# Performance work log

Measured on AMD Instinct MI355X. Metric: run time of the kernel, lower is better.

Reference implementation:

```python
import jax, jax.numpy as jnp
import numpy as np

B, D = 8192, 8          # batch, number of input features (= number of TT cores)
P = 10                  # poly_deg + 1 (basis width per feature)
R = 512                 # fixed TT rank
OUT = 64                # output dim (dims[0])
N_MID = D - 2           # middle cores
U_LO, U_HI = -0.1, 0.1  # uniform init range


def setup_inputs() -> dict:
    key = jax.random.key(0)
    kz, k0, km, kl = jax.random.split(key, 4)
    z = jax.random.normal(kz, (B, D), dtype=jnp.float32)
    G0 = jax.random.uniform(k0, (P, R), minval=U_LO, maxval=U_HI, dtype=jnp.float32)
    G_mid = jax.random.uniform(km, (N_MID, R, P, R), minval=U_LO, maxval=U_HI, dtype=jnp.float32)
    G_last = jax.random.uniform(kl, (R, P, OUT), minval=U_LO, maxval=U_HI, dtype=jnp.float32)
    return {"z": z, "G0": G0, "G_mid": G_mid, "G_last": G_last, "t": 0}


def _poly_basis(z, p):
    # Phi[i] = [z_i^0, ..., z_i^(p-1)]  -> stacked as [B, D, P]
    return z[:, :, None] ** jnp.arange(p, dtype=z.dtype)


def reference(z, G0, G_mid, G_last, t):
    phi = _poly_basis(z, G0.shape[0])                 # [B, D, P]
    # first core: tanh(G0)[j, r], Phi0[b, j] -> res[b, r]
    res = jnp.einsum('jr,bj->br', jnp.tanh(G0), phi[:, 0, :])
    # middle cores: res[b,i] . tanh(G)[i,j,k] . Phi[b,j] -> [b,k]
    for i in range(G_mid.shape[0]):
        tmp = jnp.einsum('bi,ijk->bjk', res, jnp.tanh(G_mid[i]))   # [B, P, R]
        res = jnp.einsum('bjk,bj->bk', tmp, phi[:, i + 1, :])      # [B, R]
    # last core -> output dim
    tmp = jnp.einsum('bi,ijl->bjl', res, jnp.tanh(G_last))         # [B, P, OUT]
    res = jnp.einsum('bjl,bj->bl', tmp, phi[:, -1, :])             # [B, OUT]
    return res
```

## Files before the change

kernel.cpp:

```cpp
#include <hip/hip_runtime.h>
#include <hip/hip_bf16.h>
#include <stdint.h>

#define BB   8192
#define DD   8
#define PP   10
#define RR   512
#define OUTD 64
#define KK   5120

typedef __bf16 bf16x8 __attribute__((ext_vector_type(8)));
typedef float  f32x4  __attribute__((ext_vector_type(4)));

template <int N>
__global__ __launch_bounds__(256) void frag_pack(
        const float* __restrict__ G, __hip_bfloat16* __restrict__ dst, int ldi) {
    constexpr int LOGN = (N == 512) ? 9 : 6;
    __shared__ __hip_bfloat16 sT[32 * (N + 8)];
    const int kc = blockIdx.x, j = blockIdx.y, c = blockIdx.z;
    const float* Gp = G + (size_t)c * 512 * ldi;
    __hip_bfloat16* db = dst + (size_t)c * 5120 * N + (size_t)(j * 16 + kc) * 32 * N;
    #pragma unroll
    for (int e = 0; e < N / 32; ++e) {
        const int idx = (e * 256 + threadIdx.x) * 4;
        const int row = idx >> LOGN, col = idx & (N - 1);
        f32x4 v = *(const f32x4*)(Gp + (size_t)(kc * 32 + row) * ldi + (size_t)j * N + col);
        __hip_bfloat16* sp = sT + row * (N + 8) + col;
        sp[0] = __float2bfloat16(tanhf(v.x));
        sp[1] = __float2bfloat16(tanhf(v.y));
        sp[2] = __float2bfloat16(tanhf(v.z));
        sp[3] = __float2bfloat16(tanhf(v.w));
    }
    __syncthreads();
    #pragma unroll
    for (int cc = 0; cc < N / 64; ++cc) {
        const int ch = cc * 256 + threadIdx.x;
        const int nt = ch >> 6, l = ch & 63;
        const int r0 = (l >> 4) * 8, cb = nt * 16 + (l & 15);
        union { __hip_bfloat16 h[8]; uint4 u; } pk;
        #pragma unroll
        for (int e = 0; e < 8; ++e) pk.h[e] = sT[(r0 + e) * (N + 8) + cb];
        *(uint4*)(db + (size_t)ch * 8) = pk.u;
    }
}

__global__ __launch_bounds__(512) void tanh_g0(
        const float* __restrict__ G0, float* __restrict__ tG0) {
    const int i = blockIdx.x * 512 + threadIdx.x;
    tG0[i] = tanhf(G0[i]);
}

__global__ __launch_bounds__(512) void tt_first(
        const float* __restrict__ z, const float* __restrict__ tG0,
        __hip_bfloat16* __restrict__ res0) {
    const int r = threadIdx.x;
    const int b0 = blockIdx.x * 32;
    float tg[10];
    #pragma unroll
    for (int j = 0; j < 10; ++j) tg[j] = tG0[j * RR + r];
    #pragma unroll 1
    for (int b = 0; b < 32; ++b) {
        const float z0 = z[(size_t)(b0 + b) * DD];
        float acc = tg[9];
        #pragma unroll
        for (int j = 8; j >= 0; --j) acc = acc * z0 + tg[j];
        res0[(size_t)(b0 + b) * RR + r] = __float2bfloat16(acc);
    }
}

template <bool LASTV, int NTOT>
__global__ __launch_bounds__(256, 2) void tt_gemm_ks(
        const __hip_bfloat16* __restrict__ resin,
        const __hip_bfloat16* __restrict__ tBf,
        void* __restrict__ outp,
        const float* __restrict__ z, int d) {
    __shared__ f32x4 red[2][16][64];

    const int tid  = threadIdx.x;
    const int lane = tid & 63;
    const int wave = tid >> 6;
    const int m0 = blockIdx.x * 64;
    const int nb = blockIdx.y;
    const int r16 = lane & 15, quad = lane >> 4;

    bf16x8 a[16];
    #pragma unroll
    for (int ms = 0; ms < 4; ++ms)
        #pragma unroll
        for (int kst = 0; kst < 4; ++kst)
            a[ms * 4 + kst] = *(const bf16x8*)(
                resin + (size_t)(m0 + ms * 16 + r16) * RR + wave * 128 + kst * 32 + quad * 8);

    float zr[16];
    #pragma unroll
    for (int ms = 0; ms < 4; ++ms)
        #pragma unroll
        for (int r = 0; r < 4; ++r)
            zr[ms * 4 + r] = z[(size_t)(m0 + ms * 16 + quad * 4 + r) * DD + d];

    f32x4 acc[4][4];
    #pragma unroll
    for (int ms = 0; ms < 4; ++ms)
        #pragma unroll
        for (int sn = 0; sn < 4; ++sn) acc[ms][sn] = f32x4{0.f, 0.f, 0.f, 0.f};

    constexpr size_t SK = (size_t)NTOT * 512;
    constexpr size_t PJ = 16 * SK;
    const __hip_bfloat16* pB = tBf + (size_t)nb * 4 * 512
                             + (size_t)wave * 4 * SK + (size_t)lane * 8;

    bf16x8 bv[4][4];
    #pragma unroll
    for (int s = 0; s < 3; ++s)
        #pragma unroll
        for (int sn = 0; sn < 4; ++sn)
            bv[s][sn] = *(const bf16x8*)(pB + (size_t)9 * PJ + (size_t)s * SK + sn * 512);

#define MFMA_STEP(SLOT)                                                        \
    _Pragma("unroll")                                                          \
    for (int ms = 0; ms < 4; ++ms)                                             \
        _Pragma("unroll")                                                      \
        for (int sn = 0; sn < 4; ++sn)                                         \
            acc[ms][sn] = __builtin_amdgcn_mfma_f32_16x16x32_bf16(             \
                a[ms * 4 + SLOT], bv[SLOT][sn], acc[ms][sn], 0, 0, 0);

    #pragma unroll 1
    for (int p = 0; p < 10; ++p) {
        const int j = 9 - p;
        if (p) {
            #pragma unroll
            for (int ms = 0; ms < 4; ++ms)
                #pragma unroll
                for (int sn = 0; sn < 4; ++sn)
                    #pragma unroll
                    for (int r = 0; r < 4; ++r)
                        acc[ms][sn][r] *= zr[ms * 4 + r];
        }
        const size_t jb = (size_t)j * PJ;
        #pragma unroll
        for (int sn = 0; sn < 4; ++sn)
            bv[3][sn] = *(const bf16x8*)(pB + jb + (size_t)3 * SK + sn * 512);
        MFMA_STEP(0)
        if (p < 9) {
            #pragma unroll
            for (int sn = 0; sn < 4; ++sn)
                bv[0][sn] = *(const bf16x8*)(pB + jb - PJ + sn * 512);
        }
        MFMA_STEP(1)
        if (p < 9) {
            #pragma unroll
            for (int sn = 0; sn < 4; ++sn)
                bv[1][sn] = *(const bf16x8*)(pB + jb - PJ + SK + sn * 512);
        }
        MFMA_STEP(2)
        if (p < 9) {
            #pragma unroll
            for (int sn = 0; sn < 4; ++sn)
                bv[2][sn] = *(const bf16x8*)(pB + jb - PJ + 2 * SK + sn * 512);
        }
        MFMA_STEP(3)
    }
#undef MFMA_STEP

    if (wave & 1) {
        const int idx = wave >> 1;
        #pragma unroll
        for (int i = 0; i < 16; ++i) red[idx][i][lane] = acc[i >> 2][i & 3];
    }
    __syncthreads();
    if (wave == 0) {
        #pragma unroll
        for (int i = 0; i < 16; ++i) acc[i >> 2][i & 3] += red[0][i][lane];
    }
    if (wave == 2) {
        #pragma unroll
        for (int i = 0; i < 16; ++i) {
            f32x4 t = acc[i >> 2][i & 3] + red[1][i][lane];
            red[1][i][lane] = t;
        }
    }
    __syncthreads();
    float* rc = (float*)&red[0][0][0];
    if (wave == 0) {
        #pragma unroll
        for (int i = 0; i < 16; ++i) acc[i >> 2][i & 3] += red[1][i][lane];
        #pragma unroll
        for (int ms = 0; ms < 4; ++ms)
            #pragma unroll
            for (int sn = 0; sn < 4; ++sn)
                #pragma unroll
                for (int r = 0; r < 4; ++r)
                    rc[(ms * 16 + quad * 4 + r) * 64 + sn * 16 + r16] = acc[ms][sn][r];
    }
    __syncthreads();

    const int row = tid >> 2, cg = (tid & 3) * 16;
    if (LASTV) {
        float* o = (float*)outp;
        #pragma unroll
        for (int q = 0; q < 4; ++q)
            *(f32x4*)(o + (size_t)(m0 + row) * OUTD + cg + q * 4) =
                *(const f32x4*)(rc + row * 64 + cg + q * 4);
    } else {
        __hip_bfloat16* o = (__hip_bfloat16*)outp;
        #pragma unroll
        for (int h = 0; h < 2; ++h) {
            union { __hip_bfloat16 hh[8]; uint4 u; } pk;
            #pragma unroll
            for (int e = 0; e < 8; ++e)
                pk.hh[e] = __float2bfloat16(rc[row * 64 + cg + h * 8 + e]);
            *(uint4*)(o + (size_t)(m0 + row) * RR + nb * 64 + cg + h * 8) = pk.u;
        }
    }
}

extern "C" void kernel_launch(void* const* d_in, const int* in_sizes, int n_in,
                              void* d_out, int out_size, void* d_ws, size_t ws_size,
                              hipStream_t stream) {
    const float* z     = (const float*)d_in[0];
    const float* G0    = (const float*)d_in[1];
    const float* Gmid  = (const float*)d_in[2];
    const float* Glast = (const float*)d_in[3];
    float* out = (float*)d_out;

    char* ws = (char*)d_ws;
    __hip_bfloat16* resX   = (__hip_bfloat16*)ws;
    __hip_bfloat16* resY   = (__hip_bfloat16*)(ws + ((size_t)8 << 20));
    __hip_bfloat16* tBf    = (__hip_bfloat16*)(ws + ((size_t)16 << 20));
    __hip_bfloat16* tBlf   = (__hip_bfloat16*)(ws + ((size_t)48 << 20));
    float* tG0             = (float*)(ws + ((size_t)52 << 20));

    frag_pack<512><<<dim3(16, 10, 6), 256, 0, stream>>>(Gmid,  tBf,  PP * RR);
    frag_pack<64> <<<dim3(16, 10, 1), 256, 0, stream>>>(Glast, tBlf, PP * OUTD);
    tanh_g0<<<dim3(10), 512, 0, stream>>>(G0, tG0);
    tt_first<<<dim3(BB / 32), 512, 0, stream>>>(z, tG0, resX);

    __hip_bfloat16* rin = resX;
    __hip_bfloat16* rnext = resY;
    for (int c = 0; c < 6; ++c) {
        tt_gemm_ks<false, 32><<<dim3(BB / 64, RR / 64), 256, 0, stream>>>(
            rin, tBf + (size_t)c * RR * KK, rnext, z, c + 1);
        __hip_bfloat16* t = rin; rin = rnext; rnext = t;
    }
    tt_gemm_ks<true, 4><<<dim3(BB / 64, 1), 256, 0, stream>>>(
        rin, tBlf, out, z, 7);
}
```

Measured before the change: 388.5 us.

## Fuse all stages into one persistent kernel with atomic grid barriers

Replaces the ten separate launches (weight packing, tanh of G0, first core, six middle GEMMs, last GEMM) with a single persistent kernel of 512 blocks that uses atomic-counter grid barriers between stages. Each block now computes two N-tiles per middle core instead of one block per tile, and the last core is split into 16-row tiles across all blocks. This removes launch gaps and per-kernel ramp-up and tail time. In exchange it relies on all 512 blocks being co-resident (2 per CU), adds barrier spin costs, and halves the parallel tiles in flight per stage.

```diff
diff --git a/kernel.cpp b/kernel.cpp
--- a/kernel.cpp
+++ b/kernel.cpp
@@ -8,113 +8,187 @@
 #define RR   512
 #define OUTD 64
 #define KK   5120
+#define NBLK 512
 
 typedef __bf16 bf16x8 __attribute__((ext_vector_type(8)));
 typedef float  f32x4  __attribute__((ext_vector_type(4)));
 
-template <int N>
-__global__ __launch_bounds__(256) void frag_pack(
-        const float* __restrict__ G, __hip_bfloat16* __restrict__ dst, int ldi) {
-    constexpr int LOGN = (N == 512) ? 9 : 6;
-    __shared__ __hip_bfloat16 sT[32 * (N + 8)];
-    const int kc = blockIdx.x, j = blockIdx.y, c = blockIdx.z;
-    const float* Gp = G + (size_t)c * 512 * ldi;
-    __hip_bfloat16* db = dst + (size_t)c * 5120 * N + (size_t)(j * 16 + kc) * 32 * N;
-    #pragma unroll
-    for (int e = 0; e < N / 32; ++e) {
-        const int idx = (e * 256 + threadIdx.x) * 4;
-        const int row = idx >> LOGN, col = idx & (N - 1);
-        f32x4 v = *(const f32x4*)(Gp + (size_t)(kc * 32 + row) * ldi + (size_t)j * N + col);
-        __hip_bfloat16* sp = sT + row * (N + 8) + col;
-        sp[0] = __float2bfloat16(tanhf(v.x));
-        sp[1] = __float2bfloat16(tanhf(v.y));
-        sp[2] = __float2bfloat16(tanhf(v.z));
-        sp[3] = __float2bfloat16(tanhf(v.w));
+__device__ __forceinline__ void grid_sync(int* cnt, int idx) {
+    __syncthreads();
+    if (threadIdx.x == 0) {
+        __threadfence();
+        __hip_atomic_fetch_add(cnt + idx, 1, __ATOMIC_RELEASE,
+                               __HIP_MEMORY_SCOPE_AGENT);
+        int tries = 0;
+        while (__hip_atomic_load(cnt + idx, __ATOMIC_ACQUIRE,
+                                 __HIP_MEMORY_SCOPE_AGENT) < NBLK
+               && tries < (1 << 24)) {
+            __builtin_amdgcn_s_sleep(2);
+            ++tries;
+        }
+        __threadfence();
     }
     __syncthreads();
-    #pragma unroll
-    for (int cc = 0; cc < N / 64; ++cc) {
-        const int ch = cc * 256 + threadIdx.x;
-        const int nt = ch >> 6, l = ch & 63;
-        const int r0 = (l >> 4) * 8, cb = nt * 16 + (l & 15);
-        union { __hip_bfloat16 h[8]; uint4 u; } pk;
-        #pragma unroll
-        for (int e = 0; e < 8; ++e) pk.h[e] = sT[(r0 + e) * (N + 8) + cb];
-        *(uint4*)(db + (size_t)ch * 8) = pk.u;
-    }
 }
 
-__global__ __launch_bounds__(512) void tanh_g0(
-        const float* __restrict__ G0, float* __restrict__ tG0) {
-    const int i = blockIdx.x * 512 + threadIdx.x;
-    tG0[i] = tanhf(G0[i]);
-}
-
-__global__ __launch_bounds__(512) void tt_first(
-        const float* __restrict__ z, const float* __restrict__ tG0,
-        __hip_bfloat16* __restrict__ res0) {
-    const int r = threadIdx.x;
-    const int b0 = blockIdx.x * 32;
-    float tg[10];
-    #pragma unroll
-    for (int j = 0; j < 10; ++j) tg[j] = tG0[j * RR + r];
-    #pragma unroll 1
-    for (int b = 0; b < 32; ++b) {
-        const float z0 = z[(size_t)(b0 + b) * DD];
-        float acc = tg[9];
-        #pragma unroll
-        for (int j = 8; j >= 0; --j) acc = acc * z0 + tg[j];
-        res0[(size_t)(b0 + b) * RR + r] = __float2bfloat16(acc);
-    }
-}
-
-template <bool LASTV, int NTOT>
-__global__ __launch_bounds__(256, 2) void tt_gemm_ks(
-        const __hip_bfloat16* __restrict__ resin,
-        const __hip_bfloat16* __restrict__ tBf,
-        void* __restrict__ outp,
-        const float* __restrict__ z, int d) {
-    __shared__ f32x4 red[2][16][64];
-
+__global__ __launch_bounds__(256, 2) void tt_mega(
+        const float* __restrict__ z, const float* __restrict__ G0,
+        const float* __restrict__ Gmid, const float* __restrict__ Glast,
+        float* __restrict__ out,
+        __hip_bfloat16* resX, __hip_bfloat16* resY,
+        __hip_bfloat16* tBf, __hip_bfloat16* tBlf,
+        float* tG0, int* cnt) {
+    __shared__ char smraw[33280] __attribute__((aligned(16)));
+
+    const int bid  = blockIdx.x;
     const int tid  = threadIdx.x;
     const int lane = tid & 63;
     const int wave = tid >> 6;
-    const int m0 = blockIdx.x * 64;
-    const int nb = blockIdx.y;
-    const int r16 = lane & 15, quad = lane >> 4;
-
-    bf16x8 a[16];
-    #pragma unroll
-    for (int ms = 0; ms < 4; ++ms)
+    const int r16  = lane & 15;
+    const int quad = lane >> 4;
+
+    {
+        __hip_bfloat16* sT = (__hip_bfloat16*)smraw;
+        #pragma unroll 1
+        for (int u = bid; u < 970; u += NBLK) {
+            __syncthreads();
+            if (u < 960) {
+                const int c = u / 160, rem = u - c * 160;
+                const int j = rem >> 4, kc = rem & 15;
+                const float* Gp = Gmid + (size_t)c * (512 * 5120);
+                __hip_bfloat16* db = tBf + (size_t)c * (RR * KK)
+                                   + (size_t)(j * 16 + kc) * 16384;
+                #pragma unroll
+                for (int e = 0; e < 16; ++e) {
+                    const int idx = (e * 256 + tid) * 4;
+                    const int row = idx >> 9, col = idx & 511;
+                    f32x4 v = *(const f32x4*)(Gp + (size_t)(kc * 32 + row) * 5120
+                                              + (size_t)j * 512 + col);
+                    __hip_bfloat16* sp = sT + row * 520 + col;
+                    sp[0] = __float2bfloat16(tanhf(v.x));
+                    sp[1] = __float2bfloat16(tanhf(v.y));
+                    sp[2] = __float2bfloat16(tanhf(v.z));
+                    sp[3] = __float2bfloat16(tanhf(v.w));
+                }
+                __syncthreads();
+                #pragma unroll
+                for (int cc = 0; cc < 8; ++cc) {
+                    const int ch = cc * 256 + tid;
+                    const int nt = ch >> 6, l = ch & 63;
+                    const int r0 = (l >> 4) * 8, cb = nt * 16 + (l & 15);
+                    union { __hip_bfloat16 h[8]; uint4 u4; } pk;
+                    #pragma unroll
+                    for (int e = 0; e < 8; ++e) pk.h[e] = sT[(r0 + e) * 520 + cb];
+                    *(uint4*)(db + (size_t)ch * 8) = pk.u4;
+                }
+            } else {
+                const int j = u - 960;
+                #pragma unroll 1
+                for (int kc = 0; kc < 16; ++kc) {
+                    __syncthreads();
+                    #pragma unroll
+                    for (int it = 0; it < 2; ++it) {
+                        const int idx = (it * 256 + tid) * 4;
+                        const int row = idx >> 6, col = idx & 63;
+                        f32x4 v = *(const f32x4*)(Glast
+                                   + (size_t)(kc * 32 + row) * 640
+                                   + (size_t)j * 64 + col);
+                        __hip_bfloat16* sp = sT + row * 72 + col;
+                        sp[0] = __float2bfloat16(tanhf(v.x));
+                        sp[1] = __float2bfloat16(tanhf(v.y));
+                        sp[2] = __float2bfloat16(tanhf(v.z));
+                        sp[3] = __float2bfloat16(tanhf(v.w));
+                    }
+                    __syncthreads();
+                    {
+                        const int ch = tid;
+                        const int nt = ch >> 6, l = ch & 63;
+                        const int r0 = (l >> 4) * 8, cb = nt * 16 + (l & 15);
+                        union { __hip_bfloat16 h[8]; uint4 u4; } pk;
+                        #pragma unroll
+                        for (int e = 0; e < 8; ++e) pk.h[e] = sT[(r0 + e) * 72 + cb];
+                        *(uint4*)(tBlf + (size_t)(j * 16 + kc) * 2048
+                                  + (size_t)ch * 8) = pk.u4;
+                    }
+                }
+            }
+        }
+        if (bid == 458) {
+            for (int x = tid; x < 5120; x += 256) tG0[x] = tanhf(G0[x]);
+        }
+    }
+    grid_sync(cnt, 0);
+
+    {
+        const int g = bid * 256 + tid;
+        const int r = g & 511;
+        const int brow = g >> 9;
+        float tg[10];
         #pragma unroll
-        for (int kst = 0; kst < 4; ++kst)
-            a[ms * 4 + kst] = *(const bf16x8*)(
-                resin + (size_t)(m0 + ms * 16 + r16) * RR + wave * 128 + kst * 32 + quad * 8);
-
-    float zr[16];
-    #pragma unroll
-    for (int ms = 0; ms < 4; ++ms)
-        #pragma unroll
-        for (int r = 0; r < 4; ++r)
-            zr[ms * 4 + r] = z[(size_t)(m0 + ms * 16 + quad * 4 + r) * DD + d];
-
-    f32x4 acc[4][4];
-    #pragma unroll
-    for (int ms = 0; ms < 4; ++ms)
-        #pragma unroll
-        for (int sn = 0; sn < 4; ++sn) acc[ms][sn] = f32x4{0.f, 0.f, 0.f, 0.f};
-
-    constexpr size_t SK = (size_t)NTOT * 512;
-    constexpr size_t PJ = 16 * SK;
-    const __hip_bfloat16* pB = tBf + (size_t)nb * 4 * 512
-                             + (size_t)wave * 4 * SK + (size_t)lane * 8;
-
-    bf16x8 bv[4][4];
-    #pragma unroll
-    for (int s = 0; s < 3; ++s)
-        #pragma unroll
-        for (int sn = 0; sn < 4; ++sn)
-            bv[s][sn] = *(const bf16x8*)(pB + (size_t)9 * PJ + (size_t)s * SK + sn * 512);
+        for (int j = 0; j < 10; ++j) tg[j] = tG0[j * 512 + r];
+        #pragma unroll 1
+        for (int it = 0; it < 32; ++it) {
+            const int b = brow + it * 256;
+            const float z0 = z[(size_t)b * DD];
+            float acc = tg[9];
+            #pragma unroll
+            for (int j = 8; j >= 0; --j) acc = acc * z0 + tg[j];
+            resX[(size_t)b * RR + r] = __float2bfloat16(acc);
+        }
+    }
+    grid_sync(cnt, 1);
+
+    {
+        f32x4* redp = (f32x4*)smraw;
+        float* rc   = (float*)smraw;
+        constexpr size_t SKM = 16384;
+        constexpr size_t PJM = 16 * SKM;
+        const int m0  = (bid & 127) * 64;
+        const int nbb = bid >> 7;
+
+        #pragma unroll 1
+        for (int c = 0; c < 6; ++c) {
+            const __hip_bfloat16* rin  = (c & 1) ? resY : resX;
+            __hip_bfloat16*       rout = (c & 1) ? resX : resY;
+            const __hip_bfloat16* tB = tBf + (size_t)c * (RR * KK);
+            const int d = c + 1;
+
+            bf16x8 a[16];
+            #pragma unroll
+            for (int ms = 0; ms < 4; ++ms)
+                #pragma unroll
+                for (int kst = 0; kst < 4; ++kst)
+                    a[ms * 4 + kst] = *(const bf16x8*)(
+                        rin + (size_t)(m0 + ms * 16 + r16) * RR
+                        + wave * 128 + kst * 32 + quad * 8);
+
+            float zr[16];
+            #pragma unroll
+            for (int ms = 0; ms < 4; ++ms)
+                #pragma unroll
+                for (int r = 0; r < 4; ++r)
+                    zr[ms * 4 + r] = z[(size_t)(m0 + ms * 16 + quad * 4 + r) * DD + d];
+
+            #pragma unroll 1
+            for (int h = 0; h < 2; ++h) {
+                const int nb = nbb + h * 4;
+                f32x4 acc[4][4];
+                #pragma unroll
+                for (int ms = 0; ms < 4; ++ms)
+                    #pragma unroll
+                    for (int sn = 0; sn < 4; ++sn)
+                        acc[ms][sn] = f32x4{0.f, 0.f, 0.f, 0.f};
+
+                const __hip_bfloat16* pB = tB + (size_t)nb * 2048
+                                         + (size_t)wave * 4 * SKM
+                                         + (size_t)lane * 8;
+                bf16x8 bv[4][4];
+                #pragma unroll
+                for (int s = 0; s < 3; ++s)
+                    #pragma unroll
+                    for (int sn = 0; sn < 4; ++sn)
+                        bv[s][sn] = *(const bf16x8*)(pB + (size_t)9 * PJM
+                                                     + (size_t)s * SKM + sn * 512);
 
 #define MFMA_STEP(SLOT)                                                        \
     _Pragma("unroll")                                                          \
@@ -124,92 +198,201 @@
             acc[ms][sn] = __builtin_amdgcn_mfma_f32_16x16x32_bf16(             \
                 a[ms * 4 + SLOT], bv[SLOT][sn], acc[ms][sn], 0, 0, 0);
 
-    #pragma unroll 1
-    for (int p = 0; p < 10; ++p) {
-        const int j = 9 - p;
-        if (p) {
-            #pragma unroll
-            for (int ms = 0; ms < 4; ++ms)
+                #pragma unroll 1
+                for (int p = 0; p < 10; ++p) {
+                    const int j = 9 - p;
+                    if (p) {
+                        #pragma unroll
+                        for (int ms = 0; ms < 4; ++ms)
+                            #pragma unroll
+                            for (int sn = 0; sn < 4; ++sn)
+                                #pragma unroll
+                                for (int r = 0; r < 4; ++r)
+                                    acc[ms][sn][r] *= zr[ms * 4 + r];
+                    }
+                    const size_t jb = (size_t)j * PJM;
+                    #pragma unroll
+                    for (int sn = 0; sn < 4; ++sn)
+                        bv[3][sn] = *(const bf16x8*)(pB + jb + (size_t)3 * SKM + sn * 512);
+                    MFMA_STEP(0)
+                    if (p < 9) {
+                        #pragma unroll
+                        for (int sn = 0; sn < 4; ++sn)
+                            bv[0][sn] = *(const bf16x8*)(pB + jb - PJM + sn * 512);
+                    }
+                    MFMA_STEP(1)
+                    if (p < 9) {
+                        #pragma unroll
+                        for (int sn = 0; sn < 4; ++sn)
+                            bv[1][sn] = *(const bf16x8*)(pB + jb - PJM + SKM + sn * 512);
+                    }
+                    MFMA_STEP(2)
+                    if (p < 9) {
+                        #pragma unroll
+                        for (int sn = 0; sn < 4; ++sn)
+                            bv[2][sn] = *(const bf16x8*)(pB + jb - PJM + 2 * SKM + sn * 512);
+                    }
+                    MFMA_STEP(3)
+                }
+#undef MFMA_STEP
+
+                __syncthreads();
+                if (wave & 1) {
+                    const int idx = wave >> 1;
+                    #pragma unroll
+                    for (int i = 0; i < 16; ++i)
+                        redp[idx * 1024 + i * 64 + lane] = acc[i >> 2][i & 3];
+                }
+                __syncthreads();
+                if (wave == 0) {
+                    #pragma unroll
+                    for (int i = 0; i < 16; ++i)
+                        acc[i >> 2][i & 3] += redp[i * 64 + lane];
+                }
+                if (wave == 2) {
+                    #pragma unroll
+                    for (int i = 0; i < 16; ++i) {
+                        f32x4 t = acc[i >> 2][i & 3] + redp[1024 + i * 64 + lane];
+                        redp[1024 + i * 64 + lane] = t;
+                    }
+                }
+                __syncthreads();
+                if (wave == 0) {
+                    #pragma unroll
+                    for (int i = 0; i < 16; ++i)
+                        acc[i >> 2][i & 3] += redp[1024 + i * 64 + lane];
+                    #pragma unroll
+                    for (int ms = 0; ms < 4; ++ms)
+                        #pragma unroll
+                        for (int sn = 0; sn < 4; ++sn)
+                            #pragma unroll
+                            for (int r = 0; r < 4; ++r)
+                                rc[(ms * 16 + quad * 4 + r) * 64 + sn * 16 + r16] =
+                                    acc[ms][sn][r];
+                }
+                __syncthreads();
+                {
+                    const int row = tid >> 2, cg = (tid & 3) * 16;
+                    #pragma unroll
+                    for (int hh = 0; hh < 2; ++hh) {
+                        union { __hip_bfloat16 h8[8]; uint4 u4; } pk;
+                        #pragma unroll
+                        for (int e = 0; e < 8; ++e)
+                            pk.h8[e] = __float2bfloat16(rc[row * 64 + cg + hh * 8 + e]);
+                        *(uint4*)(rout + (size_t)(m0 + row) * RR
+                                  + nb * 64 + cg + hh * 8) = pk.u4;
+                    }
+                }
+            }
+            grid_sync(cnt, 2 + c);
+        }
+    }
+
+    {
+        f32x4* redp = (f32x4*)smraw;
+        float* rc   = (float*)smraw;
+        constexpr size_t SKL = 2048, PJL = 16 * SKL;
+        const int m0 = bid * 16;
+        const __hip_bfloat16* rin = resX;
+
+        bf16x8 a2[4];
+        #pragma unroll
+        for (int kst = 0; kst < 4; ++kst)
+            a2[kst] = *(const bf16x8*)(rin + (size_t)(m0 + r16) * RR
+                                       + wave * 128 + kst * 32 + quad * 8);
+        float zl[4];
+        #pragma unroll
+        for (int r = 0; r < 4; ++r)
+            zl[r] = z[(size_t)(m0 + quad * 4 + r) * DD + 7];
+
+        f32x4 acc1[4];
+        #pragma unroll
+        for (int sn = 0; sn < 4; ++sn) acc1[sn] = f32x4{0.f, 0.f, 0.f, 0.f};
+
+        const __hip_bfloat16* pB = tBlf + (size_t)wave * 4 * SKL + (size_t)lane * 8;
+        bf16x8 bv[4][4];
+        #pragma unroll
+        for (int s = 0; s < 3; ++s)
+            #pragma unroll
+            for (int sn = 0; sn < 4; ++sn)
+                bv[s][sn] = *(const bf16x8*)(pB + (size_t)9 * PJL
+                                             + (size_t)s * SKL + sn * 512);
+
+#define MFMA_STEPL(SLOT)                                                       \
+    _Pragma("unroll")                                                          \
+    for (int sn = 0; sn < 4; ++sn)                                             \
+        acc1[sn] = __builtin_amdgcn_mfma_f32_16x16x32_bf16(                    \
+            a2[SLOT], bv[SLOT][sn], acc1[sn], 0, 0, 0);
+
+        #pragma unroll 1
+        for (int p = 0; p < 10; ++p) {
+            const int j = 9 - p;
+            if (p) {
                 #pragma unroll
                 for (int sn = 0; sn < 4; ++sn)
                     #pragma unroll
                     for (int r = 0; r < 4; ++r)
-                        acc[ms][sn][r] *= zr[ms * 4 + r];
-        }
-        const size_t jb = (size_t)j * PJ;
-        #pragma unroll
-        for (int sn = 0; sn < 4; ++sn)
-            bv[3][sn] = *(const bf16x8*)(pB + jb + (size_t)3 * SK + sn * 512);
-        MFMA_STEP(0)
-        if (p < 9) {
+                        acc1[sn][r] *= zl[r];
+            }
+            const size_t jb = (size_t)j * PJL;
             #pragma unroll
             for (int sn = 0; sn < 4; ++sn)
-                bv[0][sn] = *(const bf16x8*)(pB + jb - PJ + sn * 512);
-        }
-        MFMA_STEP(1)
-        if (p < 9) {
+                bv[3][sn] = *(const bf16x8*)(pB + jb + (size_t)3 * SKL + sn * 512);
+            MFMA_STEPL(0)
+            if (p < 9) {
+                #pragma unroll
+                for (int sn = 0; sn < 4; ++sn)
+                    bv[0][sn] = *(const bf16x8*)(pB + jb - PJL + sn * 512);
+            }
+            MFMA_STEPL(1)
+            if (p < 9) {
+                #pragma unroll
+                for (int sn = 0; sn < 4; ++sn)
+                    bv[1][sn] = *(const bf16x8*)(pB + jb - PJL + SKL + sn * 512);
+            }
+            MFMA_STEPL(2)
+            if (p < 9) {
+                #pragma unroll
+                for (int sn = 0; sn < 4; ++sn)
+                    bv[2][sn] = *(const bf16x8*)(pB + jb - PJL + 2 * SKL + sn * 512);
+            }
+            MFMA_STEPL(3)
+        }
+#undef MFMA_STEPL
+
+        __syncthreads();
+        if (wave & 1) {
+            const int idx = wave >> 1;
+            #pragma unroll
+            for (int i = 0; i < 4; ++i) redp[idx * 256 + i * 64 + lane] = acc1[i];
+        }
+        __syncthreads();
+        if (wave == 0) {
+            #pragma unroll
+            for (int i = 0; i < 4; ++i) acc1[i] += redp[i * 64 + lane];
+        }
+        if (wave == 2) {
+            #pragma unroll
+            for (int i = 0; i < 4; ++i) {
+                f32x4 t = acc1[i] + redp[256 + i * 64 + lane];
+                redp[256 + i * 64 + lane] = t;
+            }
+        }
+        __syncthreads();
+        if (wave == 0) {
+            #pragma unroll
+            for (int i = 0; i < 4; ++i) acc1[i] += redp[256 + i * 64 + lane];
             #pragma unroll
             for (int sn = 0; sn < 4; ++sn)
-                bv[1][sn] = *(const bf16x8*)(pB + jb - PJ + SK + sn * 512);
-        }
-        MFMA_STEP(2)
-        if (p < 9) {
-            #pragma unroll
-            for (int sn = 0; sn < 4; ++sn)
-                bv[2][sn] = *(const bf16x8*)(pB + jb - PJ + 2 * SK + sn * 512);
-        }
-        MFMA_STEP(3)
-    }
-#undef MFMA_STEP
-
-    if (wave & 1) {
-        const int idx = wave >> 1;
-        #pragma unroll
-        for (int i = 0; i < 16; ++i) red[idx][i][lane] = acc[i >> 2][i & 3];
-    }
-    __syncthreads();
-    if (wave == 0) {
-        #pragma unroll
-        for (int i = 0; i < 16; ++i) acc[i >> 2][i & 3] += red[0][i][lane];
-    }
-    if (wave == 2) {
-        #pragma unroll
-        for (int i = 0; i < 16; ++i) {
-            f32x4 t = acc[i >> 2][i & 3] + red[1][i][lane];
-            red[1][i][lane] = t;
-        }
-    }
-    __syncthreads();
-    float* rc = (float*)&red[0][0][0];
-    if (wave == 0) {
-        #pragma unroll
-        for (int i = 0; i < 16; ++i) acc[i >> 2][i & 3] += red[1][i][lane];
-        #pragma unroll
-        for (int ms = 0; ms < 4; ++ms)
-            #pragma unroll
-            for (int sn = 0; sn < 4; ++sn)
                 #pragma unroll
                 for (int r = 0; r < 4; ++r)
-                    rc[(ms * 16 + quad * 4 + r) * 64 + sn * 16 + r16] = acc[ms][sn][r];
-    }
-    __syncthreads();
-
-    const int row = tid >> 2, cg = (tid & 3) * 16;
-    if (LASTV) {
-        float* o = (float*)outp;
-        #pragma unroll
-        for (int q = 0; q < 4; ++q)
-            *(f32x4*)(o + (size_t)(m0 + row) * OUTD + cg + q * 4) =
-                *(const f32x4*)(rc + row * 64 + cg + q * 4);
-    } else {
-        __hip_bfloat16* o = (__hip_bfloat16*)outp;
-        #pragma unroll
-        for (int h = 0; h < 2; ++h) {
-            union { __hip_bfloat16 hh[8]; uint4 u; } pk;
-            #pragma unroll
-            for (int e = 0; e < 8; ++e)
-                pk.hh[e] = __float2bfloat16(rc[row * 64 + cg + h * 8 + e]);
-            *(uint4*)(o + (size_t)(m0 + row) * RR + nb * 64 + cg + h * 8) = pk.u;
+                    rc[(quad * 4 + r) * 64 + sn * 16 + r16] = acc1[sn][r];
+        }
+        __syncthreads();
+        {
+            const int row = tid >> 4, col = (tid & 15) * 4;
+            *(f32x4*)(out + (size_t)(m0 + row) * OUTD + col) =
+                *(const f32x4*)(rc + row * 64 + col);
         }
     }
 }
@@ -224,24 +407,14 @@
     float* out = (float*)d_out;
 
     char* ws = (char*)d_ws;
-    __hip_bfloat16* resX   = (__hip_bfloat16*)ws;
-    __hip_bfloat16* resY   = (__hip_bfloat16*)(ws + ((size_t)8 << 20));
-    __hip_bfloat16* tBf    = (__hip_bfloat16*)(ws + ((size_t)16 << 20));
-    __hip_bfloat16* tBlf   = (__hip_bfloat16*)(ws + ((size_t)48 << 20));
-    float* tG0             = (float*)(ws + ((size_t)52 << 20));
-
-    frag_pack<512><<<dim3(16, 10, 6), 256, 0, stream>>>(Gmid,  tBf,  PP * RR);
-    frag_pack<64> <<<dim3(16, 10, 1), 256, 0, stream>>>(Glast, tBlf, PP * OUTD);
-    tanh_g0<<<dim3(10), 512, 0, stream>>>(G0, tG0);
-    tt_first<<<dim3(BB / 32), 512, 0, stream>>>(z, tG0, resX);
-
-    __hip_bfloat16* rin = resX;
-    __hip_bfloat16* rnext = resY;
-    for (int c = 0; c < 6; ++c) {
-        tt_gemm_ks<false, 32><<<dim3(BB / 64, RR / 64), 256, 0, stream>>>(
-            rin, tBf + (size_t)c * RR * KK, rnext, z, c + 1);
-        __hip_bfloat16* t = rin; rin = rnext; rnext = t;
-    }
-    tt_gemm_ks<true, 4><<<dim3(BB / 64, 1), 256, 0, stream>>>(
-        rin, tBlf, out, z, 7);
+    __hip_bfloat16* resX = (__hip_bfloat16*)ws;
+    __hip_bfloat16* resY = (__hip_bfloat16*)(ws + ((size_t)8 << 20));
+    __hip_bfloat16* tBf  = (__hip_bfloat16*)(ws + ((size_t)16 << 20));
+    __hip_bfloat16* tBlf = (__hip_bfloat16*)(ws + ((size_t)48 << 20));
+    float* tG0           = (float*)(ws + ((size_t)49 << 20));
+    int* cnt             = (int*)(ws + ((size_t)50 << 20));
+
+    hipMemsetAsync(cnt, 0, 64, stream);
+    tt_mega<<<dim3(NBLK), dim3(256), 0, stream>>>(
+        z, G0, Gmid, Glast, out, resX, resY, tBf, tBlf, tG0, cnt);
 }
```

New measurement: 991.0 us. 155% more time.
